# Performance work log

Measured on AMD Instinct MI355X. Metric: run time of the kernel, lower is better.

## Reference

```python
import jax, jax.numpy as jnp
import numpy as np

WS = 7          # window size
NH = 16         # n_heads
DIM = 512
HEAD_DIM = DIM // NH
SCALE = HEAD_DIM ** -0.5


def _rel_pos_index(ws):
    coords = np.stack(np.meshgrid(np.arange(ws), np.arange(ws), indexing='ij'))  # [2,ws,ws]
    coords = coords.reshape(2, -1)                                               # [2,N]
    rel = coords[:, :, None] - coords[:, None, :]                                # [2,N,N]
    idx = (rel[0] + ws - 1) * (2 * ws - 1) + (rel[1] + ws - 1)                   # [N,N]
    return jnp.asarray(idx, dtype=jnp.int32)


def _window_partition(x, ws):
    B, H, W, C = x.shape
    x = x.reshape(B, H // ws, ws, W // ws, ws, C)
    x = x.transpose(0, 1, 3, 2, 4, 5)
    return x.reshape(-1, ws * ws, C)  # [B*nW, N, C]


def setup_inputs() -> dict:
    key = jax.random.key(0)
    k1, k2, k3 = jax.random.split(key, 3)
    qkv = jax.random.normal(k1, (3, 32, 56, 56, DIM), dtype=jnp.float32)
    mask = jax.random.normal(k2, (64, WS * WS, WS * WS), dtype=jnp.float32)
    bias_table = jax.random.normal(k3, ((2 * WS - 1) ** 2, NH), dtype=jnp.float32) * 0.02
    return {"qkv": qkv, "mask": mask, "bias_table": bias_table}


def reference(qkv, mask, bias_table):
    q, k, v = qkv[0], qkv[1], qkv[2]
    B, H, W, C = q.shape
    N = WS * WS
    # window partition + split heads -> [BS, NH, N, HEAD_DIM]
    def prep(x):
        x = _window_partition(x, WS)                       # [BS, N, C]
        BS = x.shape[0]
        return x.reshape(BS, N, NH, HEAD_DIM).transpose(0, 2, 1, 3)
    q, k, v = prep(q), prep(k), prep(v)
    BS = q.shape[0]

    attn = jnp.einsum('bhnd,bhmd->bhnm', q, k) * SCALE      # [BS, NH, N, N]

    idx = _rel_pos_index(WS)                                # [N, N] static
    rel_bias = bias_table[idx]                              # [N, N, NH]
    attn = attn + rel_bias.transpose(2, 0, 1)[None]         # [BS, NH, N, N]

    nW = mask.shape[0]
    attn = attn.reshape(BS // nW, nW, NH, N, N) + mask[None, :, None]
    attn = attn.reshape(BS, NH, N, N)

    attn = jax.nn.softmax(attn, axis=-1)
    x = jnp.einsum('bhnm,bhmd->bhnd', attn, v)              # [BS, NH, N, HEAD_DIM]
    return x.transpose(0, 2, 1, 3).reshape(BS, N, C)
```

## Files before the change

### kernel.cpp

```cpp
#include <hip/hip_runtime.h>

#define NTOK 49
#define NH 16
#define DIM 512
#define HD 32
#define HPB 4
#define SCALE 0.17677669529663687f

typedef __attribute__((ext_vector_type(8))) short short8;
typedef __attribute__((ext_vector_type(16))) float f32x16;

__device__ __forceinline__ unsigned short f2b(float x) {
    union { float f; unsigned u; } v; v.f = x;
    unsigned u = v.u;
    u += 0x7fffu + ((u >> 16) & 1u);
    return (unsigned short)(u >> 16);
}

__device__ __forceinline__ unsigned long long pack4(float4 v) {
    unsigned lo = (unsigned)f2b(v.x) | ((unsigned)f2b(v.y) << 16);
    unsigned hi = (unsigned)f2b(v.z) | ((unsigned)f2b(v.w) << 16);
    return (unsigned long long)lo | ((unsigned long long)hi << 32);
}

__device__ __forceinline__ short8 pack8(float4 a, float4 b) {
    short8 r;
    r[0] = (short)f2b(a.x); r[1] = (short)f2b(a.y);
    r[2] = (short)f2b(a.z); r[3] = (short)f2b(a.w);
    r[4] = (short)f2b(b.x); r[5] = (short)f2b(b.y);
    r[6] = (short)f2b(b.z); r[7] = (short)f2b(b.w);
    return r;
}

__global__ __launch_bounds__(256, 4) void winattn_mfma(
    const float* __restrict__ qkv,
    const float* __restrict__ mask,
    const float* __restrict__ bias_table,
    float* __restrict__ out)
{
    __shared__ __align__(16) unsigned short Vr[HPB][64][32];
    __shared__ float maskl[NTOK * NTOK];
    __shared__ float biasl[HPB][176];
    __shared__ float invl[HPB][64];

    const int bx   = blockIdx.x;
    const int win  = bx >> 2;
    const int hg   = bx & 3;
    const int tid  = threadIdx.x;
    const int wave = tid >> 6;
    const int lane = tid & 63;
    const int ln   = lane & 31;
    const int h    = lane >> 5;
    const int head0 = hg * HPB;
    const int head  = head0 + wave;

    const int b  = win >> 6;
    const int w  = win & 63;
    const int wr = w >> 3, wc = w & 7;

    const size_t plane = (size_t)32 * 56 * 56 * 512;

    for (int e = tid; e < HPB * 64 * 8; e += 256) {
        const int hh = e >> 9;
        const int t  = (e >> 3) & 63;
        const int d4 = e & 7;
        unsigned long long vz = 0;
        if (t < NTOK) {
            const int i = t / 7, j = t - i * 7;
            const size_t goff = (((size_t)(b * 56 + wr * 7 + i)) * 56 + (wc * 7 + j)) * 512
                              + (head0 + hh) * HD + d4 * 4;
            vz = pack4(*(const float4*)(qkv + 2 * plane + goff));
        }
        *(unsigned long long*)&Vr[hh][t][d4 * 4] = vz;
    }
    for (int e = tid; e < NTOK * NTOK; e += 256)
        maskl[e] = mask[(size_t)w * (NTOK * NTOK) + e];
    for (int e = tid; e < 169 * HPB; e += 256) {
        const int hh = e / 169, r = e - hh * 169;
        biasl[hh][r] = bias_table[r * NH + head0 + hh];
    }

    const int t0 = ln;
    const int t1 = (32 + ln <= 48) ? (32 + ln) : 48;
    const size_t wbase = (((size_t)(b * 56 + wr * 7)) * 56 + wc * 7) * 512 + head * HD;

    short8 qfr[2][2], kfr[2][2];
    #pragma unroll
    for (int tt = 0; tt < 2; ++tt) {
        const int t  = tt ? t1 : t0;
        const int i  = t / 7, j = t - i * 7;
        const float* qp = qkv + wbase + (size_t)(i * 56 + j) * 512 + h * 8;
        const float* kp = qp + plane;
        float4 q0 = *(const float4*)(qp);
        float4 q1 = *(const float4*)(qp + 4);
        float4 q2 = *(const float4*)(qp + 16);
        float4 q3 = *(const float4*)(qp + 20);
        float4 k0 = *(const float4*)(kp);
        float4 k1 = *(const float4*)(kp + 4);
        float4 k2 = *(const float4*)(kp + 16);
        float4 k3 = *(const float4*)(kp + 20);
        qfr[tt][0] = pack8(q0, q1);  qfr[tt][1] = pack8(q2, q3);
        kfr[tt][0] = pack8(k0, k1);  kfr[tt][1] = pack8(k2, k3);
    }

    __syncthreads();

    f32x16 zer;
    #pragma unroll
    for (int i = 0; i < 16; ++i) zer[i] = 0.f;
    f32x16 acc[2][2];
    acc[0][0] = zer; acc[0][1] = zer; acc[1][0] = zer; acc[1][1] = zer;
    #pragma unroll
    for (int ks = 0; ks < 2; ++ks) {
        acc[0][0] = __builtin_amdgcn_mfma_f32_32x32x16_bf16(kfr[0][ks], qfr[0][ks], acc[0][0], 0, 0, 0);
        acc[0][1] = __builtin_amdgcn_mfma_f32_32x32x16_bf16(kfr[0][ks], qfr[1][ks], acc[0][1], 0, 0, 0);
        acc[1][0] = __builtin_amdgcn_mfma_f32_32x32x16_bf16(kfr[1][ks], qfr[0][ks], acc[1][0], 0, 0, 0);
        acc[1][1] = __builtin_amdgcn_mfma_f32_32x32x16_bf16(kfr[1][ks], qfr[1][ks], acc[1][1], 0, 0, 0);
    }

    unsigned wpk[2][2][8];
    #pragma unroll
    for (int nt = 0; nt < 2; ++nt) {
        const int n  = 32 * nt + ln;
        const int nc = n < NTOK ? n : NTOK - 1;
        const int i_n = nc / 7;
        const int tn  = nc + 6 * i_n + 84;
        float pl[2][16];
        float mx = -3.0e38f;
        #pragma unroll
        for (int mt = 0; mt < 2; ++mt) {
            #pragma unroll
            for (int r = 0; r < 16; ++r) {
                const int mb  = 32 * mt + (r & 3) + 8 * (r >> 2);
                const int m0  = mb, m1 = mb + 4;
                const int mc0 = m0 < NTOK ? m0 : NTOK - 1;
                const int mc1 = m1 < NTOK ? m1 : NTOK - 1;
                const int tm0 = mc0 + 6 * (mc0 / 7);
                const int tm1 = mc1 + 6 * (mc1 / 7);
                const int mc  = h ? mc1 : mc0;
                const int tm  = h ? tm1 : tm0;
                float s = acc[mt][nt][r] * SCALE + biasl[wave][tn - tm] + maskl[nc * NTOK + mc];
                const bool dead = h ? (m1 >= NTOK) : (m0 >= NTOK);
                s = dead ? -3.0e38f : s;
                pl[mt][r] = s;
                mx = fmaxf(mx, s);
            }
        }
        mx = fmaxf(mx, __shfl_xor(mx, 32));
        float sum = 0.f;
        #pragma unroll
        for (int mt = 0; mt < 2; ++mt) {
            #pragma unroll
            for (int g = 0; g < 8; ++g) {
                const int ia = (g < 4) ? g : g + 4;
                const float e0 = __expf(pl[mt][ia] - mx);
                const float e1 = __expf(pl[mt][ia + 4] - mx);
                sum += e0 + e1;
                wpk[nt][mt][g] = (unsigned)f2b(e0) | ((unsigned)f2b(e1) << 16);
            }
        }
        sum += __shfl_xor(sum, 32);
        if (h == 0 && n < NTOK)
            invl[wave][n] = 1.0f / sum;
    }

    f32x16 oacc[2];
    oacc[0] = zer; oacc[1] = zer;
    #pragma unroll
    for (int ksv = 0; ksv < 4; ++ksv) {
        short8 vf;
        #pragma unroll
        for (int j = 0; j < 8; ++j)
            vf[j] = (short)Vr[wave][16 * ksv + 8 * h + j][ln];
        const int mt = ksv >> 1;
        #pragma unroll
        for (int nt = 0; nt < 2; ++nt) {
            unsigned short alo[4], ahi[4];
            #pragma unroll
            for (int jj = 0; jj < 4; ++jj) {
                const unsigned W = wpk[nt][mt][(ksv & 1) * 4 + jj];
                const unsigned U = (unsigned)__shfl_xor((int)W, 32);
                alo[jj] = h ? (unsigned short)(U >> 16) : (unsigned short)(W & 0xffffu);
                ahi[jj] = h ? (unsigned short)(W >> 16) : (unsigned short)(U & 0xffffu);
            }
            short8 af;
            af[0] = (short)alo[0]; af[1] = (short)alo[1];
            af[2] = (short)alo[2]; af[3] = (short)alo[3];
            af[4] = (short)ahi[0]; af[5] = (short)ahi[1];
            af[6] = (short)ahi[2]; af[7] = (short)ahi[3];
            oacc[nt] = __builtin_amdgcn_mfma_f32_32x32x16_bf16(af, vf, oacc[nt], 0, 0, 0);
        }
    }

    const size_t obase = ((size_t)win * NTOK) * DIM + head * HD + ln;
    #pragma unroll
    for (int nt = 0; nt < 2; ++nt) {
        #pragma unroll
        for (int r = 0; r < 16; ++r) {
            const int nb = 32 * nt + (r & 3) + 8 * (r >> 2);
            const int n  = h ? nb + 4 : nb;
            if (n < NTOK)
                out[obase + (size_t)n * DIM] = oacc[nt][r] * invl[wave][n];
        }
    }
}

extern "C" void kernel_launch(void* const* d_in, const int* in_sizes, int n_in,
                              void* d_out, int out_size, void* d_ws, size_t ws_size,
                              hipStream_t stream) {
    const float* qkv        = (const float*)d_in[0];
    const float* mask       = (const float*)d_in[1];
    const float* bias_table = (const float*)d_in[2];
    float* out = (float*)d_out;

    const int nblocks = 2048 * (NH / HPB);
    winattn_mfma<<<nblocks, 256, 0, stream>>>(qkv, mask, bias_table, out);
}
```

Before: 198.7 us.

## Make each wave stage its own V, mask and bias to drop block barrier

Each wave now loads and converts its own head's V tile, a private copy of the window mask (stored as bf16) and its bias row into LDS. This removes the block-wide __syncthreads, so waves no longer wait on one another. The softmax scale is folded into Q before the bf16 conversion, which drops a multiply per score. In exchange, mask global reads are repeated by four waves per block, LDS use for the mask grows, and storing the mask in bf16 reduces its precision.

```diff
diff --git a/kernel.cpp b/kernel.cpp
--- a/kernel.cpp
+++ b/kernel.cpp
@@ -10,6 +10,8 @@
 typedef __attribute__((ext_vector_type(8))) short short8;
 typedef __attribute__((ext_vector_type(16))) float f32x16;
 
+struct __attribute__((packed, aligned(4))) f4u { float x, y, z, w; };
+
 __device__ __forceinline__ unsigned short f2b(float x) {
     union { float f; unsigned u; } v; v.f = x;
     unsigned u = v.u;
@@ -17,18 +19,23 @@
     return (unsigned short)(u >> 16);
 }
 
+__device__ __forceinline__ float b2f(unsigned short b) {
+    union { unsigned u; float f; } v; v.u = ((unsigned)b) << 16;
+    return v.f;
+}
+
 __device__ __forceinline__ unsigned long long pack4(float4 v) {
     unsigned lo = (unsigned)f2b(v.x) | ((unsigned)f2b(v.y) << 16);
     unsigned hi = (unsigned)f2b(v.z) | ((unsigned)f2b(v.w) << 16);
     return (unsigned long long)lo | ((unsigned long long)hi << 32);
 }
 
-__device__ __forceinline__ short8 pack8(float4 a, float4 b) {
+__device__ __forceinline__ short8 pack8s(float4 a, float4 b, float sc) {
     short8 r;
-    r[0] = (short)f2b(a.x); r[1] = (short)f2b(a.y);
-    r[2] = (short)f2b(a.z); r[3] = (short)f2b(a.w);
-    r[4] = (short)f2b(b.x); r[5] = (short)f2b(b.y);
-    r[6] = (short)f2b(b.z); r[7] = (short)f2b(b.w);
+    r[0] = (short)f2b(a.x * sc); r[1] = (short)f2b(a.y * sc);
+    r[2] = (short)f2b(a.z * sc); r[3] = (short)f2b(a.w * sc);
+    r[4] = (short)f2b(b.x * sc); r[5] = (short)f2b(b.y * sc);
+    r[6] = (short)f2b(b.z * sc); r[7] = (short)f2b(b.w * sc);
     return r;
 }
 
@@ -39,8 +46,8 @@
     float* __restrict__ out)
 {
     __shared__ __align__(16) unsigned short Vr[HPB][64][32];
-    __shared__ float maskl[NTOK * NTOK];
-    __shared__ float biasl[HPB][176];
+    __shared__ __align__(8)  unsigned short maskw[HPB][2404];
+    __shared__ float biasw[HPB][176];
     __shared__ float invl[HPB][64];
 
     const int bx   = blockIdx.x;
@@ -51,59 +58,71 @@
     const int lane = tid & 63;
     const int ln   = lane & 31;
     const int h    = lane >> 5;
-    const int head0 = hg * HPB;
-    const int head  = head0 + wave;
+    const int head = hg * HPB + wave;
 
     const int b  = win >> 6;
     const int w  = win & 63;
     const int wr = w >> 3, wc = w & 7;
 
     const size_t plane = (size_t)32 * 56 * 56 * 512;
-
-    for (int e = tid; e < HPB * 64 * 8; e += 256) {
-        const int hh = e >> 9;
-        const int t  = (e >> 3) & 63;
-        const int d4 = e & 7;
-        unsigned long long vz = 0;
-        if (t < NTOK) {
-            const int i = t / 7, j = t - i * 7;
-            const size_t goff = (((size_t)(b * 56 + wr * 7 + i)) * 56 + (wc * 7 + j)) * 512
-                              + (head0 + hh) * HD + d4 * 4;
-            vz = pack4(*(const float4*)(qkv + 2 * plane + goff));
-        }
-        *(unsigned long long*)&Vr[hh][t][d4 * 4] = vz;
-    }
-    for (int e = tid; e < NTOK * NTOK; e += 256)
-        maskl[e] = mask[(size_t)w * (NTOK * NTOK) + e];
-    for (int e = tid; e < 169 * HPB; e += 256) {
-        const int hh = e / 169, r = e - hh * 169;
-        biasl[hh][r] = bias_table[r * NH + head0 + hh];
-    }
+    const size_t wbase = (((size_t)(b * 56 + wr * 7)) * 56 + wc * 7) * 512 + head * HD;
 
     const int t0 = ln;
     const int t1 = (32 + ln <= 48) ? (32 + ln) : 48;
-    const size_t wbase = (((size_t)(b * 56 + wr * 7)) * 56 + wc * 7) * 512 + head * HD;
-
-    short8 qfr[2][2], kfr[2][2];
+    float4 qv[2][4], kv[2][4];
     #pragma unroll
     for (int tt = 0; tt < 2; ++tt) {
         const int t  = tt ? t1 : t0;
         const int i  = t / 7, j = t - i * 7;
         const float* qp = qkv + wbase + (size_t)(i * 56 + j) * 512 + h * 8;
         const float* kp = qp + plane;
-        float4 q0 = *(const float4*)(qp);
-        float4 q1 = *(const float4*)(qp + 4);
-        float4 q2 = *(const float4*)(qp + 16);
-        float4 q3 = *(const float4*)(qp + 20);
-        float4 k0 = *(const float4*)(kp);
-        float4 k1 = *(const float4*)(kp + 4);
-        float4 k2 = *(const float4*)(kp + 16);
-        float4 k3 = *(const float4*)(kp + 20);
-        qfr[tt][0] = pack8(q0, q1);  qfr[tt][1] = pack8(q2, q3);
-        kfr[tt][0] = pack8(k0, k1);  kfr[tt][1] = pack8(k2, k3);
-    }
-
-    __syncthreads();
+        qv[tt][0] = *(const float4*)(qp);
+        qv[tt][1] = *(const float4*)(qp + 4);
+        qv[tt][2] = *(const float4*)(qp + 16);
+        qv[tt][3] = *(const float4*)(qp + 20);
+        kv[tt][0] = *(const float4*)(kp);
+        kv[tt][1] = *(const float4*)(kp + 4);
+        kv[tt][2] = *(const float4*)(kp + 16);
+        kv[tt][3] = *(const float4*)(kp + 20);
+    }
+
+    #pragma unroll
+    for (int e = 0; e < 8; ++e) {
+        const int idx = e * 64 + lane;
+        const int t   = idx >> 3;
+        const int d4  = idx & 7;
+        unsigned long long vz = 0;
+        if (t < NTOK) {
+            const int i = t / 7, j = t - i * 7;
+            vz = pack4(*(const float4*)(qkv + 2 * plane + wbase
+                                        + (size_t)(i * 56 + j) * 512 + d4 * 4));
+        }
+        *(unsigned long long*)&Vr[wave][t][d4 * 4] = vz;
+    }
+
+    const float* mrow = mask + (size_t)w * 2401;
+    for (int e = lane; e < 600; e += 64) {
+        f4u mv = *(const f4u*)(mrow + 4 * e);
+        unsigned long long pk =
+              (unsigned long long)f2b(mv.x)
+            | ((unsigned long long)f2b(mv.y) << 16)
+            | ((unsigned long long)f2b(mv.z) << 32)
+            | ((unsigned long long)f2b(mv.w) << 48);
+        *(unsigned long long*)&maskw[wave][4 * e] = pk;
+    }
+    if (lane == 0) maskw[wave][2400] = f2b(mrow[2400]);
+
+    for (int r = lane; r < 169; r += 64)
+        biasw[wave][r] = bias_table[r * NH + head];
+
+    short8 qfr[2][2], kfr[2][2];
+    #pragma unroll
+    for (int tt = 0; tt < 2; ++tt) {
+        qfr[tt][0] = pack8s(qv[tt][0], qv[tt][1], SCALE);
+        qfr[tt][1] = pack8s(qv[tt][2], qv[tt][3], SCALE);
+        kfr[tt][0] = pack8s(kv[tt][0], kv[tt][1], 1.0f);
+        kfr[tt][1] = pack8s(kv[tt][2], kv[tt][3], 1.0f);
+    }
 
     f32x16 zer;
     #pragma unroll
@@ -139,7 +158,8 @@
                 const int tm1 = mc1 + 6 * (mc1 / 7);
                 const int mc  = h ? mc1 : mc0;
                 const int tm  = h ? tm1 : tm0;
-                float s = acc[mt][nt][r] * SCALE + biasl[wave][tn - tm] + maskl[nc * NTOK + mc];
+                float s = acc[mt][nt][r] + biasw[wave][tn - tm]
+                        + b2f(maskw[wave][nc * NTOK + mc]);
                 const bool dead = h ? (m1 >= NTOK) : (m0 >= NTOK);
                 s = dead ? -3.0e38f : s;
                 pl[mt][r] = s;
```

Measured after the change: 197.4 us. About the same (-0.7%).
